# Optimization experiments

Measured on AMD Instinct MI355X. Metric: run time of the kernel, lower is better.

The kernel has to match this reference:

```python
import jax, jax.numpy as jnp
import numpy as np

N, E, B, H, F = 20000, 400000, 200, 10, 78
HID = H * F  # 780
SEQ, VOC, EMB, NF, KS = 1000, 26, 128, 32, 8
CONV_OUT = SEQ - KS + 1  # 993


def setup_inputs() -> dict:
    key = jax.random.key(0)
    ks = jax.random.split(key, 40)
    g = lambda i, shape, s=0.05: jax.random.normal(ks[i], shape, jnp.float32) * s
    inp = {
        "x": jax.random.normal(ks[0], (N, F), jnp.float32),
        "edge_index": jax.random.randint(ks[1], (2, E), 0, N),
        "batch": jnp.sort(jax.random.randint(ks[2], (N,), 0, B)),
        "target": jax.random.randint(ks[3], (B, SEQ), 0, VOC),
        # GATConv(78 -> 78, heads=10)
        "gat_W": g(4, (F, HID)),
        "gat_a_src": g(5, (H, F)),
        "gat_a_dst": g(6, (H, F)),
        "gat_b": g(7, (HID,)),
        # GCNConv(780 -> 780)
        "gcn_W": g(8, (HID, HID)),
        "gcn_b": g(9, (HID,)),
        # graph MLP head
        "fcg1_W": g(10, (HID, 1500)), "fcg1_b": g(11, (1500,)),
        "fcg2_W": g(12, (1500, 128)), "fcg2_b": g(13, (128,)),
        # protein branch
        "emb": g(14, (VOC, EMB)),
        "cW": g(15, (NF, EMB, KS)), "cb": g(16, (NF,)),
        "fxt_W": g(17, (NF * CONV_OUT, 128)), "fxt_b": g(18, (128,)),
        # fusion MLP
        "f1_W": g(19, (256, 1024)), "f1_b": g(20, (1024,)),
        "f2_W": g(21, (1024, 512)), "f2_b": g(22, (512,)),
        "f3_W": g(23, (512, 256)), "f3_b": g(24, (256,)),
        "f4_W": g(25, (256, 128)), "f4_b": g(26, (128,)),
        "o_W": g(27, (128, 1)), "o_b": g(28, (1,)),
    }
    return inp


def _graph_branch(x, edge_index, batch, gat_W, gat_a_src, gat_a_dst, gat_b,
                  gcn_W, gcn_b, fcg1_W, fcg1_b, fcg2_W, fcg2_b):
    n = x.shape[0]
    loops = jnp.arange(n)
    src = jnp.concatenate([edge_index[0], loops])  # add self loops (PyG default)
    dst = jnp.concatenate([edge_index[1], loops])
    # --- GATConv ---
    h = (x @ gat_W).reshape(n, H, F)  # [N,H,F]
    a_s = jnp.einsum("nhf,hf->nh", h, gat_a_src)
    a_d = jnp.einsum("nhf,hf->nh", h, gat_a_dst)
    e = jax.nn.leaky_relu(a_s[src] + a_d[dst], 0.2)  # [Etot,H]
    m = jax.ops.segment_max(e, dst, num_segments=n)
    ex = jnp.exp(e - m[dst])
    den = jax.ops.segment_sum(ex, dst, num_segments=n)
    alpha = ex / den[dst]
    agg = jax.ops.segment_sum(h[src] * alpha[:, :, None], dst, num_segments=n)
    x1 = jax.nn.relu(agg.reshape(n, HID) + gat_b)
    # --- GCNConv (sym norm with self loops) ---
    deg = jax.ops.segment_sum(jnp.ones_like(dst, jnp.float32), dst, num_segments=n)
    dinv = jax.lax.rsqrt(jnp.maximum(deg, 1.0))
    norm = dinv[src] * dinv[dst]
    h2 = x1 @ gcn_W
    x2 = jax.ops.segment_sum(h2[src] * norm[:, None], dst, num_segments=n) + gcn_b
    x2 = jax.nn.relu(x2)
    # --- global add pool + MLP ---
    xg = jax.ops.segment_sum(x2, batch, num_segments=B)
    xg = jax.nn.relu(xg @ fcg1_W + fcg1_b)  # dropout = identity (eval)
    return xg @ fcg2_W + fcg2_b


def _protein_branch(target, emb, cW, cb, fxt_W, fxt_b):
    et = emb[target]  # [B,SEQ,EMB]
    c = jax.lax.conv_general_dilated(
        et.transpose(0, 2, 1), cW, (1,), "VALID",
        dimension_numbers=("NCH", "OIH", "NCH"))  # [B,NF,993]
    c = c + cb[None, :, None]
    return c.reshape(c.shape[0], NF * CONV_OUT) @ fxt_W + fxt_b


def reference(x, edge_index, batch, target, gat_W, gat_a_src, gat_a_dst, gat_b,
              gcn_W, gcn_b, fcg1_W, fcg1_b, fcg2_W, fcg2_b, emb, cW, cb,
              fxt_W, fxt_b, f1_W, f1_b, f2_W, f2_b, f3_W, f3_b, f4_W, f4_b,
              o_W, o_b):
    xg = _graph_branch(x, edge_index, batch, gat_W, gat_a_src, gat_a_dst, gat_b,
                       gcn_W, gcn_b, fcg1_W, fcg1_b, fcg2_W, fcg2_b)
    xt = _protein_branch(target, emb, cW, cb, fxt_W, fxt_b)
    xc = jnp.concatenate([xg, xt], axis=1)  # [B,256]
    xc = jax.nn.relu(xc @ f1_W + f1_b)
    xc = jax.nn.relu(xc @ f2_W + f2_b)
    xc = jax.nn.relu(xc @ f3_W + f3_b)
    xc = jax.nn.relu(xc @ f4_W + f4_b)
    return xc @ o_W + o_b  # [B,1]
```

## Files before the change

kernel.cpp:

```cpp
#include <hip/hip_runtime.h>
#include <hip/hip_bf16.h>
#include <math.h>

typedef __hip_bfloat16 bf16;
typedef __attribute__((ext_vector_type(8))) short short8v;
typedef __attribute__((ext_vector_type(4))) float float4v;

#define NODES 20000
#define EDG   400000
#define ETOT  (EDG + NODES)
#define GB    200
#define HEADS 10
#define FD    78
#define HIDD  780
#define SEQL  1000
#define VOCS  26
#define EMBD  128
#define NFC   32
#define KSZ   8
#define COUT  993
#define KFXT  (NFC * COUT)

#define MPAD  20096
#define NPADB 896
#define KP1   96
#define KP2   800
#define HP    800
#define PNL   2
#define PF    400
#define MB2   208
#define FXT_KS 128


__device__ __forceinline__ float us2f(unsigned short u) {
  unsigned int i = ((unsigned int)u) << 16; float f; __builtin_memcpy(&f, &i, 4); return f;
}
__device__ __forceinline__ float b2f(bf16 v) { return __bfloat162float(v); }
__device__ __forceinline__ float ldany(const void* p, size_t i, int m) {
  if (m) return ((const float*)p)[i];
  return b2f(((const bf16*)p)[i]);
}
__device__ __forceinline__ bool nanf_(float v) { return v != v; }
__device__ __forceinline__ unsigned short f2us(float v) {
  bf16 b = __float2bfloat16(v); unsigned short u; __builtin_memcpy(&u, &b, 2); return u;
}

__global__ void k_detect(const void* x, int* diag) {
  int t = threadIdx.x;
  const unsigned short* u = (const unsigned short*)x;
  int hit = 0;
  for (int i = t; i < 4096; i += 256) {
    float v = us2f(u[i]);
    if (nanf_(v) || fabsf(v) > 1e6f) hit = 1;
  }
  if (hit) diag[1] = 1;
}

__global__ void k_pad_x(const void* x, bf16* xpad, const int* diag) {
  int idx = blockIdx.x * 256 + threadIdx.x;
  if (idx >= MPAD * KP1) return;
  int mode = diag[1];
  int m = idx / KP1, k = idx % KP1;
  float v = (m < NODES && k < FD) ? ldany(x, (size_t)m * FD + k, mode) : 0.f;
  xpad[idx] = __float2bfloat16(v);
}

__global__ void k_tr_gatw(const void* gw, bf16* Wt, const int* diag) {
  int idx = blockIdx.x * 256 + threadIdx.x;
  if (idx >= NPADB * KP1) return;
  int mode = diag[1];
  int n = idx / KP1, k = idx % KP1;
  float v = (n < HIDD && k < FD) ? ldany(gw, (size_t)k * HIDD + n, mode) : 0.f;
  Wt[idx] = __float2bfloat16(v);
}

__global__ void k_tr_gcnw(const void* gw, bf16* Wt, const int* diag) {
  int idx = blockIdx.x * 256 + threadIdx.x;
  if (idx >= NPADB * KP2) return;
  int mode = diag[1];
  int n = idx / KP2, k = idx % KP2;
  float v = (n < HIDD && k < HIDD) ? ldany(gw, (size_t)k * HIDD + n, mode) : 0.f;
  Wt[idx] = __float2bfloat16(v);
}

__global__ void k_zero_x1pad(bf16* x1p) {
  int i = blockIdx.x * 256 + threadIdx.x;
  if (i < (MPAD - NODES) * KP2)
    x1p[(size_t)NODES * KP2 + i] = __float2bfloat16(0.f);
}

#define MT 128
#define NT 128
#define BK 32
#define LP 40
__global__ __launch_bounds__(256) void k_gemm_mfma(const bf16* A, int lda,
                                                   const bf16* Bt, int ldb,
                                                   bf16* C, int ldc, int Ncap,
                                                   int M, int Kp) {
  __shared__ __align__(16) bf16 As[MT * LP];
  __shared__ __align__(16) bf16 Bs[NT * LP];
  int t = threadIdx.x;
  int lane = t & 63, w = t >> 6;
  int wr = (w >> 1) * 64, wc = (w & 1) * 64;
  int quad = lane >> 4, mr = lane & 15;
  int m0 = blockIdx.y * MT, n0 = blockIdx.x * NT;
  float4v acc[4][4];
#pragma unroll
  for (int i = 0; i < 4; ++i)
#pragma unroll
    for (int j = 0; j < 4; ++j) acc[i][j] = (float4v){0.f, 0.f, 0.f, 0.f};

  for (int kc = 0; kc < Kp; kc += BK) {
#pragma unroll
    for (int i = 0; i < 4; ++i) {
      int c = t + i * 256;
      int row = c >> 3, col = (c & 7) * 4;
      *(uint2*)&As[row * LP + col] =
          *(const uint2*)&A[(size_t)(m0 + row) * lda + kc + col];
      *(uint2*)&Bs[row * LP + col] =
          *(const uint2*)&Bt[(size_t)(n0 + row) * ldb + kc + col];
    }
    __syncthreads();
    short8v af[4], bfr[4];
#pragma unroll
    for (int i = 0; i < 4; ++i)
      af[i] = *(const short8v*)&As[(wr + i * 16 + mr) * LP + quad * 8];
#pragma unroll
    for (int j = 0; j < 4; ++j)
      bfr[j] = *(const short8v*)&Bs[(wc + j * 16 + mr) * LP + quad * 8];
#pragma unroll
    for (int i = 0; i < 4; ++i)
#pragma unroll
      for (int j = 0; j < 4; ++j)
        acc[i][j] = __builtin_amdgcn_mfma_f32_16x16x32_bf16(af[i], bfr[j], acc[i][j], 0, 0, 0);
    __syncthreads();
  }
#pragma unroll
  for (int i = 0; i < 4; ++i) {
    int gm0 = m0 + wr + i * 16 + quad * 4;
#pragma unroll
    for (int j = 0; j < 4; ++j) {
      int gn = n0 + wc + j * 16 + mr;
      if (gn >= Ncap) continue;
#pragma unroll
      for (int r = 0; r < 4; ++r) {
        int gm = gm0 + r;
        if (gm < M) C[(size_t)gm * ldc + gn] = __float2bfloat16(acc[i][j][r]);
      }
    }
  }
}

#define MLP_NT 64
#define MLP_BK 32
#define MLP_MT 208
#define MLP_LP 40
__global__ __launch_bounds__(256) void k_mlp_mfma(const void* A, int lda, const void* Bw,
                                                  const void* bias, float* out, int ostride,
                                                  int ooff, int M, int Nn, int K,
                                                  int ksplit, int aRelu, int aBf16,
                                                  const int* diag) {
  __shared__ __align__(16) bf16 As[MLP_MT * MLP_LP];
  __shared__ __align__(16) bf16 Bs[MLP_NT * MLP_LP];
  int mode = diag[1];
  int t = threadIdx.x;
  int lane = t & 63, w = t >> 6;
  int quad = lane >> 4, mr = lane & 15;
  int n0 = blockIdx.x * MLP_NT;
  int kz = blockIdx.y;
  int nchunks = (K + MLP_BK - 1) / MLP_BK;
  int cpk = (nchunks + ksplit - 1) / ksplit;
  int c0 = kz * cpk, c1 = c0 + cpk;
  if (c1 > nchunks) c1 = nchunks;
  float4v acc[13];
#pragma unroll
  for (int i = 0; i < 13; ++i) acc[i] = (float4v){0.f, 0.f, 0.f, 0.f};

  for (int c = c0; c < c1; ++c) {
    int k0 = c * MLP_BK;
    if (aBf16) {
      const bf16* Ab = (const bf16*)A;
      for (int e = t; e < MLP_MT * 4; e += 256) {
        int row = e >> 2, c8 = (e & 3) * 8;
        int gk = k0 + c8;
        if (row < M && gk + 7 < K) {
          *(uint4*)&As[row * MLP_LP + c8] = *(const uint4*)&Ab[(size_t)row * lda + gk];
        } else {
#pragma unroll
          for (int kk = 0; kk < 8; ++kk) {
            float v = (row < M && gk + kk < K) ? b2f(Ab[(size_t)row * lda + gk + kk]) : 0.f;
            As[row * MLP_LP + c8 + kk] = __float2bfloat16(v);
          }
        }
      }
    } else {
      const float* Af = (const float*)A;
      for (int e = t; e < MLP_MT * 8; e += 256) {
        int row = e >> 3, c4 = (e & 7) * 4;
        int gk = k0 + c4;
        float4 v4 = {0.f, 0.f, 0.f, 0.f};
        if (row < M) {
          if (gk + 3 < K) {
            v4 = *(const float4*)&Af[(size_t)row * lda + gk];
          } else {
            v4.x = (gk + 0 < K) ? Af[(size_t)row * lda + gk + 0] : 0.f;
            v4.y = (gk + 1 < K) ? Af[(size_t)row * lda + gk + 1] : 0.f;
            v4.z = (gk + 2 < K) ? Af[(size_t)row * lda + gk + 2] : 0.f;
            v4.w = (gk + 3 < K) ? Af[(size_t)row * lda + gk + 3] : 0.f;
          }
        }
        if (aRelu) {
          v4.x = fmaxf(v4.x, 0.f); v4.y = fmaxf(v4.y, 0.f);
          v4.z = fmaxf(v4.z, 0.f); v4.w = fmaxf(v4.w, 0.f);
        }
        bf16* dst = &As[row * MLP_LP + c4];
        dst[0] = __float2bfloat16(v4.x); dst[1] = __float2bfloat16(v4.y);
        dst[2] = __float2bfloat16(v4.z); dst[3] = __float2bfloat16(v4.w);
      }
    }
    for (int e = t; e < MLP_NT * MLP_BK; e += 256) {
      int k = e >> 6, col = e & 63;
      int gk = k0 + k, gn = n0 + col;
      float v = (gn < Nn && gk < K) ? ldany(Bw, (size_t)gk * Nn + gn, mode) : 0.f;
      Bs[col * MLP_LP + k] = __float2bfloat16(v);
    }
    __syncthreads();
    short8v bf = *(const short8v*)&Bs[(w * 16 + mr) * MLP_LP + quad * 8];
#pragma unroll
    for (int i = 0; i < 13; ++i) {
      short8v af = *(const short8v*)&As[(i * 16 + mr) * MLP_LP + quad * 8];
      acc[i] = __builtin_amdgcn_mfma_f32_16x16x32_bf16(af, bf, acc[i], 0, 0, 0);
    }
    __syncthreads();
  }
  int gn = n0 + w * 16 + mr;
  if (gn >= Nn) return;
  float bs = (kz == 0) ? ldany(bias, gn, mode) : 0.f;
#pragma unroll
  for (int i = 0; i < 13; ++i) {
    int gm0 = i * 16 + quad * 4;
#pragma unroll
    for (int r = 0; r < 4; ++r) {
      int gm = gm0 + r;
      if (gm >= M) break;
      float v = acc[i][r] + bs;
      float* op = &out[(size_t)gm * ostride + ooff + gn];
      if (ksplit == 1) *op = v;
      else atomicAdd(op, v);
    }
  }
}

__global__ __launch_bounds__(256) void k_fxt(const bf16* cT, const void* Bw,
                                             float* part, const int* diag) {
  __shared__ __align__(16) bf16 As[MLP_MT * MLP_LP];
  __shared__ __align__(16) bf16 Bs[MLP_NT * MLP_LP];
  int mode = diag[1];
  int t = threadIdx.x;
  int lane = t & 63, w = t >> 6;
  int quad = lane >> 4, mr = lane & 15;
  int n0 = blockIdx.x * MLP_NT;
  int kz = blockIdx.y;
  int nchunks = KFXT / MLP_BK;
  int cpk = (nchunks + FXT_KS - 1) / FXT_KS;
  int c0 = kz * cpk, c1 = c0 + cpk;
  if (c1 > nchunks) c1 = nchunks;
  float4v acc[13];
#pragma unroll
  for (int i = 0; i < 13; ++i) acc[i] = (float4v){0.f, 0.f, 0.f, 0.f};

  for (int c = c0; c < c1; ++c) {
    int k0 = c * MLP_BK;
    for (int e = t; e < 32 * 52; e += 256) {
      int kk = e / 52, bq = e % 52;
      uint2 u = *(const uint2*)&cT[(size_t)(k0 + kk) * MB2 + bq * 4];
      unsigned short* ap = (unsigned short*)As;
      int mb = bq * 4;
      ap[(mb + 0) * MLP_LP + kk] = (unsigned short)(u.x & 0xffffu);
      ap[(mb + 1) * MLP_LP + kk] = (unsigned short)(u.x >> 16);
      ap[(mb + 2) * MLP_LP + kk] = (unsigned short)(u.y & 0xffffu);
      ap[(mb + 3) * MLP_LP + kk] = (unsigned short)(u.y >> 16);
    }
    for (int e = t; e < MLP_NT * MLP_BK; e += 256) {
      int k = e >> 6, col = e & 63;
      float v = ldany(Bw, (size_t)(k0 + k) * 128 + (n0 + col), mode);
      Bs[col * MLP_LP + k] = __float2bfloat16(v);
    }
    __syncthreads();
    short8v bf = *(const short8v*)&Bs[(w * 16 + mr) * MLP_LP + quad * 8];
#pragma unroll
    for (int i = 0; i < 13; ++i) {
      short8v af = *(const short8v*)&As[(i * 16 + mr) * MLP_LP + quad * 8];
      acc[i] = __builtin_amdgcn_mfma_f32_16x16x32_bf16(af, bf, acc[i], 0, 0, 0);
    }
    __syncthreads();
  }
  int gnl = n0 + w * 16 + mr;
#pragma unroll
  for (int i = 0; i < 13; ++i) {
#pragma unroll
    for (int r = 0; r < 4; ++r) {
      int gm = i * 16 + quad * 4 + r;
      part[((size_t)kz * MB2 + gm) * 128 + gnl] = acc[i][r];
    }
  }
}

__global__ __launch_bounds__(128) void k_fxt_red(const float* part, const void* bias,
                                                 float* xc, const int* diag) {
  int gm = blockIdx.x, n = threadIdx.x;
  int mode = diag[1];
  float s = 0.f;
  for (int kz = 0; kz < FXT_KS; ++kz)
    s += part[((size_t)kz * MB2 + gm) * 128 + n];
  xc[(size_t)gm * 256 + 128 + n] = s + ldany(bias, n, mode);
}

__global__ void k_prep_ws(const void* gat_W, const void* a_src, const void* a_dst,
                          float* Ws, float* Wd, const int* diag) {
  int idx = blockIdx.x * 256 + threadIdx.x;
  if (idx >= FD * HEADS) return;
  int mode = diag[1];
  int k = idx / HEADS, hd = idx % HEADS;
  float s = 0.f, d = 0.f;
  for (int f = 0; f < FD; ++f) {
    float w = ldany(gat_W, (size_t)k * HIDD + hd * FD + f, mode);
    s += w * ldany(a_src, (size_t)hd * FD + f, mode);
    d += w * ldany(a_dst, (size_t)hd * FD + f, mode);
  }
  Ws[k * HEADS + hd] = s;
  Wd[k * HEADS + hd] = d;
}

__global__ void k_prep_mtab(const void* emb, const void* cW, float* Mtab, const int* diag) {
  int idx = blockIdx.x * 256 + threadIdx.x;
  if (idx >= NFC * KSZ * VOCS) return;
  int mode = diag[1];
  int o = idx / (KSZ * VOCS);
  int r = idx % (KSZ * VOCS);
  int k = r / VOCS, v = r % VOCS;
  float acc = 0.f;
  for (int i = 0; i < EMBD; ++i)
    acc += ldany(emb, (size_t)v * EMBD + i, mode) * ldany(cW, ((size_t)o * EMBD + i) * KSZ + k, mode);
  Mtab[idx] = acc;
}

__global__ __launch_bounds__(256) void k_asd(const void* x, const float* Ws, const float* Wd,
                                             float* a_s, float* a_d, const int* diag) {
  __shared__ unsigned short xs[256 * FD];
  __shared__ float ws_sh[FD * HEADS], wd_sh[FD * HEADS];
  int mode = diag[1];
  int nb = blockIdx.x * 256, t = threadIdx.x;
  for (int e = t; e < FD * HEADS; e += 256) { ws_sh[e] = Ws[e]; wd_sh[e] = Wd[e]; }
  for (int e = t; e < 256 * FD; e += 256) {
    int r = e / FD, c = e % FD;
    int gn = nb + r;
    float xv = (gn < NODES) ? ldany(x, (size_t)gn * FD + c, mode) : 0.f;
    xs[e] = f2us(xv);
  }
  __syncthreads();
  int n = nb + t;
  if (n >= NODES) return;
  float as[HEADS], ad[HEADS];
#pragma unroll
  for (int hd = 0; hd < HEADS; ++hd) { as[hd] = 0.f; ad[hd] = 0.f; }
  for (int f = 0; f < FD; ++f) {
    float xv = us2f(xs[t * FD + f]);
#pragma unroll
    for (int hd = 0; hd < HEADS; ++hd) {
      as[hd] += xv * ws_sh[f * HEADS + hd];
      ad[hd] += xv * wd_sh[f * HEADS + hd];
    }
  }
#pragma unroll
  for (int hd = 0; hd < HEADS; ++hd) {
    a_s[n * HEADS + hd] = as[hd];
    a_d[n * HEADS + hd] = ad[hd];
  }
}

__global__ void k_count(const int* ei, int* cnt, int* diag) {
  int e = blockIdx.x * 256 + threadIdx.x;
  if (e >= ETOT) return;
  int d = (e < EDG) ? ei[EDG + e] : (e - EDG);
  if ((unsigned)d >= NODES) { atomicOr(diag, 8192); d = 0; }
  atomicAdd(&cnt[d], 1);
}

__global__ __launch_bounds__(1024) void k_scan(const int* cnt, int* rowstart) {
  __shared__ int wsum[16];
  __shared__ int carry;
  int t = threadIdx.x;
  int lane = t & 63, wid = t >> 6;
  if (t == 0) carry = 0;
  __syncthreads();
  for (int c = 0; c < (NODES + 1023) / 1024; ++c) {
    int i = c * 1024 + t;
    int orig = (i < NODES) ? cnt[i] : 0;
    int v = orig;
#pragma unroll
    for (int off = 1; off < 64; off <<= 1) {
      int u = __shfl_up(v, off, 64);
      if (lane >= off) v += u;
    }
    if (lane == 63) wsum[wid] = v;
    __syncthreads();
    if (t == 0) {
      int s = carry;
      for (int j = 0; j < 16; ++j) { int tmp = wsum[j]; wsum[j] = s; s += tmp; }
      carry = s;
    }
    __syncthreads();
    if (i < NODES) rowstart[i] = v - orig + wsum[wid];
    __syncthreads();
  }
  if (t == 0) rowstart[NODES] = carry;
}

__global__ void k_dinv(const int* cnt, float* dinv) {
  int n = blockIdx.x * 256 + threadIdx.x;
  if (n >= NODES) return;
  int d = cnt[n];
  dinv[n] = rsqrtf((float)(d > 0 ? d : 1));
}

__global__ void k_scatter(const int* ei, const int* rowstart, int* cur, int* es_src,
                          int* diag) {
  int e = blockIdx.x * 256 + threadIdx.x;
  if (e >= ETOT) return;
  int s, d;
  if (e < EDG) { s = ei[e]; d = ei[EDG + e]; } else { s = e - EDG; d = s; }
  if ((unsigned)d >= NODES) { atomicOr(diag, 8192); d = 0; }
  if ((unsigned)s >= NODES) { atomicOr(diag, 8192); s = 0; }
  int pos = rowstart[d] + atomicAdd(&cur[d], 1);
  if ((unsigned)pos < (unsigned)ETOT) es_src[pos] = s;
  else atomicOr(diag, 1);
}

__global__ void k_csrchk(const int* cnt, const int* cur, const int* rowst, int* diag) {
  int n = blockIdx.x * 256 + threadIdx.x;
  if (n < NODES && cur[n] != cnt[n]) atomicOr(diag, 1);
  if (n == 0 && rowst[NODES] != ETOT) atomicOr(diag, 1);
}

__global__ void k_bseg(const int* batch, int* bstart, int* diag) {
  int i = blockIdx.x * 256 + threadIdx.x;
  if (i >= NODES) return;
  int bi = batch[i];
  if ((unsigned)bi >= GB) { atomicOr(diag, 8192); bi = GB - 1; }
  int bp;
  if (i == 0) bp = -1;
  else {
    bp = batch[i - 1];
    if ((unsigned)bp >= GB) bp = GB - 1;
  }
  for (int b = bp + 1; b <= bi; ++b) bstart[b] = i;
  if (i == NODES - 1)
    for (int b = bi + 1; b <= GB; ++b) bstart[b] = NODES;
}

__global__ __launch_bounds__(64) void k_alpha(const int* es_src, const int* rowst,
                                              const float* a_s, const float* a_d,
                                              float* alpha, int* diag) {
  int d = blockIdx.x, lane = threadIdx.x;
  int start = rowst[d], end = rowst[d + 1];
  float ad[HEADS];
#pragma unroll
  for (int j = 0; j < HEADS; ++j) ad[j] = a_d[d * HEADS + j];
  float mx[HEADS];
#pragma unroll
  for (int j = 0; j < HEADS; ++j) mx[j] = -INFINITY;
  for (int base = start; base < end; base += 64) {
    int ce = base + lane;
    if (ce < end) {
      int s = es_src[ce];
      if ((unsigned)s >= NODES) { atomicOr(diag, 1); s = 0; }
#pragma unroll
      for (int j = 0; j < HEADS; ++j) {
        float v = a_s[s * HEADS + j] + ad[j];
        v = v > 0.f ? v : 0.2f * v;
        mx[j] = fmaxf(mx[j], v);
      }
    }
  }
#pragma unroll
  for (int j = 0; j < HEADS; ++j)
    for (int off = 1; off < 64; off <<= 1) mx[j] = fmaxf(mx[j], __shfl_xor(mx[j], off, 64));
  float den[HEADS];
#pragma unroll
  for (int j = 0; j < HEADS; ++j) den[j] = 0.f;
  for (int base = start; base < end; base += 64) {
    int ce = base + lane;
    if (ce < end) {
      int s = es_src[ce];
      if ((unsigned)s >= NODES) s = 0;
#pragma unroll
      for (int j = 0; j < HEADS; ++j) {
        float v = a_s[s * HEADS + j] + ad[j];
        v = v > 0.f ? v : 0.2f * v;
        den[j] += expf(v - mx[j]);
      }
    }
  }
#pragma unroll
  for (int j = 0; j < HEADS; ++j)
    for (int off = 1; off < 64; off <<= 1) den[j] += __shfl_xor(den[j], off, 64);
  if (lane == 0 && (nanf_(den[0]) || nanf_(den[HEADS - 1]))) atomicOr(diag, 2);
  for (int base = start; base < end; base += 64) {
    int ce = base + lane;
    if (ce < end) {
      int s = es_src[ce];
      if ((unsigned)s >= NODES) s = 0;
#pragma unroll
      for (int j = 0; j < HEADS; ++j) {
        float v = a_s[s * HEADS + j] + ad[j];
        v = v > 0.f ? v : 0.2f * v;
        alpha[(size_t)ce * HEADS + j] = expf(v - mx[j]) / den[j];
      }
    }
  }
}

__global__ __launch_bounds__(64) void k_gatg(const int* es_src, const int* rowst,
                                             const float* alpha, const bf16* h,
                                             const void* gat_b, bf16* x1, int* diag) {
  __shared__ int ssc[64];
  __shared__ float alw[64 * HEADS];
  int bid = blockIdx.x;
  int p = bid & (PNL - 1), d = bid >> 1;
  int lane = threadIdx.x;
  int mode = diag[1];
  int start = rowst[d], end = rowst[d + 1];
  int fb = p * PF + lane * 8;
  int hr = fb / FD;
  int hA = hr > HEADS - 1 ? HEADS - 1 : hr;
  int hB = hr + 1 > HEADS - 1 ? HEADS - 1 : hr + 1;
  int bnd = (hr + 1) * FD - fb;
  float acc[8];
#pragma unroll
  for (int k = 0; k < 8; ++k) acc[k] = 0.f;
  for (int base = start; base < end; base += 64) {
    int ce = base + lane;
    if (ce < end) {
      int s = es_src[ce];
      if ((unsigned)s >= NODES) { atomicOr(diag, 1); s = 0; }
      ssc[lane] = s;
#pragma unroll
      for (int j = 0; j < HEADS; ++j) alw[lane * HEADS + j] = alpha[(size_t)ce * HEADS + j];
    }
    __syncthreads();
    int cnt2 = end - base; if (cnt2 > 64) cnt2 = 64;
    if (lane < 50) {
      for (int e = 0; e < cnt2; ++e) {
        int ss = ssc[e];
        float aA = alw[e * HEADS + hA];
        float aB = alw[e * HEADS + hB];
        uint4 u = *(const uint4*)(h + (size_t)ss * HP + fb);
        unsigned int uw[4] = {u.x, u.y, u.z, u.w};
#pragma unroll
        for (int k = 0; k < 4; ++k) {
          float wl = (2 * k < bnd) ? aA : aB;
          float wh = (2 * k + 1 < bnd) ? aA : aB;
          acc[2 * k]     += wl * us2f((unsigned short)(uw[k] & 0xffffu));
          acc[2 * k + 1] += wh * us2f((unsigned short)(uw[k] >> 16));
        }
      }
    }
    __syncthreads();
  }
  if (lane < 50) {
    if (nanf_(acc[0]) || nanf_(acc[7])) atomicOr(diag, 8);
    unsigned short o[8];
#pragma unroll
    for (int k = 0; k < 8; ++k) {
      int f = fb + k;
      float v = 0.f;
      if (f < HIDD) v = fmaxf(acc[k] + ldany(gat_b, f, mode), 0.f);
      o[k] = f2us(v);
    }
    uint4 pack;
    __builtin_memcpy(&pack, o, 16);
    *(uint4*)(x1 + (size_t)d * KP2 + fb) = pack;
  }
}

__global__ __launch_bounds__(64) void k_gcng(const int* es_src, const int* rowst,
                                             const float* dinv, const bf16* h2,
                                             const void* gcn_b, bf16* x2b, int* diag) {
  __shared__ int ssc[64];
  __shared__ float nw[64];
  int bid = blockIdx.x;
  int p = bid & (PNL - 1), d = bid >> 1;
  int lane = threadIdx.x;
  int mode = diag[1];
  int start = rowst[d], end = rowst[d + 1];
  float dd = dinv[d];
  int fb = p * PF + lane * 8;
  float acc[8];
#pragma unroll
  for (int k = 0; k < 8; ++k) acc[k] = 0.f;
  for (int base = start; base < end; base += 64) {
    int ce = base + lane;
    if (ce < end) {
      int s = es_src[ce];
      if ((unsigned)s >= NODES) { atomicOr(diag, 1); s = 0; }
      ssc[lane] = s;
      nw[lane] = dinv[s] * dd;
    }
    __syncthreads();
    int cnt2 = end - base; if (cnt2 > 64) cnt2 = 64;
    if (lane < 50) {
      for (int e = 0; e < cnt2; ++e) {
        int ss = ssc[e];
        float nv = nw[e];
        uint4 u = *(const uint4*)(h2 + (size_t)ss * HP + fb);
        unsigned int uw[4] = {u.x, u.y, u.z, u.w};
#pragma unroll
        for (int k = 0; k < 4; ++k) {
          acc[2 * k]     += nv * us2f((unsigned short)(uw[k] & 0xffffu));
          acc[2 * k + 1] += nv * us2f((unsigned short)(uw[k] >> 16));
        }
      }
    }
    __syncthreads();
  }
  if (lane < 50) {
    if (nanf_(acc[0]) || nanf_(acc[7])) atomicOr(diag, 16);
    unsigned short o[8];
#pragma unroll
    for (int k = 0; k < 8; ++k) {
      int f = fb + k;
      float v = 0.f;
      if (f < HIDD) v = fmaxf(acc[k] + ldany(gcn_b, f, mode), 0.f);
      o[k] = f2us(v);
    }
    uint4 pack;
    __builtin_memcpy(&pack, o, 16);
    *(uint4*)(x2b + (size_t)d * HP + fb) = pack;
  }
}

__global__ __launch_bounds__(256) void k_pool(const bf16* x2b, const int* bstart,
                                              float* xg_pool) {
  int b = blockIdx.x, t = threadIdx.x;
  if (t >= 195) return;
  int r0 = bstart[b], r1 = bstart[b + 1];
  int fb = t * 4;
  float4 acc = {0.f, 0.f, 0.f, 0.f};
  for (int r = r0; r < r1; ++r) {
    uint2 u = *(const uint2*)(x2b + (size_t)r * HP + fb);
    acc.x += us2f((unsigned short)(u.x & 0xffffu));
    acc.y += us2f((unsigned short)(u.x >> 16));
    acc.z += us2f((unsigned short)(u.y & 0xffffu));
    acc.w += us2f((unsigned short)(u.y >> 16));
  }
  *(float4*)&xg_pool[(size_t)b * HIDD + fb] = acc;
}

__global__ __launch_bounds__(256) void k_convT(const int* target, const float* Mtab,
                                               const void* cb, bf16* cT, int* diag) {
  __shared__ int tg[GB * 40];
  __shared__ float Mt[KSZ * VOCS];
  int tt0 = blockIdx.x * 32, o = blockIdx.y, t = threadIdx.x;
  int mode = diag[1];
  for (int e = t; e < KSZ * VOCS; e += 256)
    Mt[e] = Mtab[(o * KSZ + e / VOCS) * VOCS + (e % VOCS)];
  for (int e = t; e < GB * 40; e += 256) {
    int b = e / 40, q = e % 40;
    int pos = tt0 + q;
    int tv = (pos < SEQL) ? target[b * SEQL + pos] : 0;
    if ((unsigned)tv >= VOCS) { atomicOr(diag, 8192); tv = 0; }
    tg[e] = tv;
  }
  __syncthreads();
  float cbv = ldany(cb, o, mode);
  for (int e = t; e < 32 * MB2; e += 256) {
    int tt = e / MB2, b = e % MB2;
    int gtt = tt0 + tt;
    if (gtt >= COUT) continue;
    float acc = 0.f;
    if (b < GB) {
#pragma unroll
      for (int k = 0; k < KSZ; ++k)
        acc += Mt[k * VOCS + tg[b * 40 + tt + k]];
      acc += cbv;
      if (nanf_(acc)) atomicOr(diag, 4096);
    }
    cT[((size_t)o * COUT + gtt) * MB2 + b] = __float2bfloat16(b < GB ? acc : 0.f);
  }
}

__global__ __launch_bounds__(64) void k_out(const float* xf4, const void* o_W,
                                            const void* o_b, void* outp, const int* diag) {
  int b = blockIdx.x, lane = threadIdx.x;
  int mode = diag[1];
  float a0 = fmaxf(xf4[b * 128 + lane], 0.f);
  float a1 = fmaxf(xf4[b * 128 + 64 + lane], 0.f);
  float v = a0 * ldany(o_W, lane, mode) + a1 * ldany(o_W, 64 + lane, mode);
  for (int off = 32; off; off >>= 1) v += __shfl_down(v, off, 64);
  if (lane == 0) {
    float r = v + ldany(o_b, 0, mode);
    int dg = diag[0];
    if (dg) r = 256.f * (1 + mode) + 8.f * (float)(__ffs(dg) - 1);
    else if (nanf_(r)) r = 200.f + 100.f * mode;
    if (mode) ((float*)outp)[b] = r;
    else ((bf16*)outp)[b] = __float2bfloat16(r);
  }
}

extern "C" void kernel_launch(void* const* d_in, const int* in_sizes, int n_in,
                              void* d_out, int out_size, void* d_ws, size_t ws_size,
                              hipStream_t stream) {
  const void* x       = d_in[0];
  const int*  ei      = (const int*)d_in[1];
  const int*  batch   = (const int*)d_in[2];
  const int*  target  = (const int*)d_in[3];
  const void* gat_W   = d_in[4];
  const void* a_src   = d_in[5];
  const void* a_dst   = d_in[6];
  const void* gat_b   = d_in[7];
  const void* gcn_W   = d_in[8];
  const void* gcn_b   = d_in[9];
  const void* fcg1_W  = d_in[10];
  const void* fcg1_b  = d_in[11];
  const void* fcg2_W  = d_in[12];
  const void* fcg2_b  = d_in[13];
  const void* emb     = d_in[14];
  const void* cW      = d_in[15];
  const void* cb      = d_in[16];
  const void* fxt_W   = d_in[17];
  const void* fxt_b   = d_in[18];
  const void* f1_W    = d_in[19];
  const void* f1_b    = d_in[20];
  const void* f2_W    = d_in[21];
  const void* f2_b    = d_in[22];
  const void* f3_W    = d_in[23];
  const void* f3_b    = d_in[24];
  const void* f4_W    = d_in[25];
  const void* f4_b    = d_in[26];
  const void* o_W     = d_in[27];
  const void* o_b     = d_in[28];

  char* w = (char*)d_ws;
  size_t off = 0;
  auto alloc = [&](size_t bytes) -> void* {
    void* p = w + off;
    off = (off + bytes + 255) & ~(size_t)255;
    return p;
  };
  bf16*  h_buf   = (bf16*)alloc((size_t)NODES * HP * 2);
  bf16*  x1p     = (bf16*)alloc((size_t)MPAD * KP2 * 2);
  bf16*  xpad    = (bf16*)alloc((size_t)MPAD * KP1 * 2);
  bf16*  gatWt   = (bf16*)alloc((size_t)NPADB * KP1 * 2);
  bf16*  gcnWt   = (bf16*)alloc((size_t)NPADB * KP2 * 2);
  float* a_s     = (float*)alloc((size_t)NODES * HEADS * 4);
  float* a_d     = (float*)alloc((size_t)NODES * HEADS * 4);
  float* alpha   = (float*)alloc((size_t)ETOT * HEADS * 4);
  float* Ws      = (float*)alloc(FD * HEADS * 4);
  float* Wd      = (float*)alloc(FD * HEADS * 4);
  float* Mtab    = (float*)alloc(NFC * KSZ * VOCS * 4);
  int*   rowst   = (int*)alloc((NODES + 1) * 4);
  float* dinv    = (float*)alloc(NODES * 4);
  int*   bstart  = (int*)alloc((GB + 1) * 4);
  bf16*  cT      = (bf16*)alloc((size_t)KFXT * MB2 * 2);
  float* part    = (float*)alloc((size_t)FXT_KS * MB2 * 128 * 4);
  size_t zoff = off;
  int*   cnt     = (int*)alloc(NODES * 4);
  int*   cur     = (int*)alloc(NODES * 4);
  int*   es_src  = (int*)alloc((size_t)ETOT * 4);
  float* xg_pool = (float*)alloc((size_t)GB * HIDD * 4);
  float* xg1     = (float*)alloc((size_t)GB * 1500 * 4);
  float* xc      = (float*)alloc((size_t)GB * 256 * 4);
  float* xf1     = (float*)alloc((size_t)GB * 1024 * 4);
  float* xf2     = (float*)alloc((size_t)GB * 512 * 4);
  float* xf3     = (float*)alloc((size_t)GB * 256 * 4);
  float* xf4     = (float*)alloc((size_t)GB * 128 * 4);
  int*   diag    = (int*)alloc(2 * 4);
  size_t zlen = off - zoff;

  bf16* x2b = x1p;

  hipMemsetAsync(w + zoff, 0, zlen, stream);

  k_detect<<<1, 256, 0, stream>>>(x, diag);

  k_pad_x<<<(MPAD * KP1 + 255) / 256, 256, 0, stream>>>(x, xpad, diag);
  k_tr_gatw<<<(NPADB * KP1 + 255) / 256, 256, 0, stream>>>(gat_W, gatWt, diag);
  k_tr_gcnw<<<(NPADB * KP2 + 255) / 256, 256, 0, stream>>>(gcn_W, gcnWt, diag);
  k_zero_x1pad<<<((MPAD - NODES) * KP2 + 255) / 256, 256, 0, stream>>>(x1p);

  k_prep_ws<<<(FD * HEADS + 255) / 256, 256, 0, stream>>>(gat_W, a_src, a_dst, Ws, Wd, diag);
  k_prep_mtab<<<(NFC * KSZ * VOCS + 255) / 256, 256, 0, stream>>>(emb, cW, Mtab, diag);

  k_gemm_mfma<<<dim3(NPADB / NT, MPAD / MT), 256, 0, stream>>>(
      xpad, KP1, gatWt, KP1, h_buf, HP, HP, NODES, KP1);
  k_asd<<<(NODES + 255) / 256, 256, 0, stream>>>(x, Ws, Wd, a_s, a_d, diag);

  k_count<<<(ETOT + 255) / 256, 256, 0, stream>>>(ei, cnt, diag);
  k_scan<<<1, 1024, 0, stream>>>(cnt, rowst);
  k_dinv<<<(NODES + 255) / 256, 256, 0, stream>>>(cnt, dinv);
  k_scatter<<<(ETOT + 255) / 256, 256, 0, stream>>>(ei, rowst, cur, es_src, diag);
  k_csrchk<<<(NODES + 255) / 256, 256, 0, stream>>>(cnt, cur, rowst, diag);
  k_bseg<<<(NODES + 255) / 256, 256, 0, stream>>>(batch, bstart, diag);

  k_alpha<<<NODES, 64, 0, stream>>>(es_src, rowst, a_s, a_d, alpha, diag);
  k_gatg<<<NODES * PNL, 64, 0, stream>>>(es_src, rowst, alpha, h_buf, gat_b, x1p, diag);

  k_gemm_mfma<<<dim3(NPADB / NT, MPAD / MT), 256, 0, stream>>>(
      x1p, KP2, gcnWt, KP2, h_buf, HP, HP, NODES, KP2);

  k_gcng<<<NODES * PNL, 64, 0, stream>>>(es_src, rowst, dinv, h_buf, gcn_b, x2b, diag);
  k_pool<<<GB, 256, 0, stream>>>(x2b, bstart, xg_pool);

  k_convT<<<dim3((COUT + 31) / 32, NFC), 256, 0, stream>>>(target, Mtab, cb, cT, diag);
  k_fxt<<<dim3(2, FXT_KS), 256, 0, stream>>>(cT, fxt_W, part, diag);
  k_fxt_red<<<GB, 128, 0, stream>>>(part, fxt_b, xc, diag);

  k_mlp_mfma<<<dim3(24, 4), 256, 0, stream>>>(xg_pool, HIDD, fcg1_W, fcg1_b,
                                              xg1, 1500, 0, GB, 1500, HIDD, 4, 0, 0, diag);
  k_mlp_mfma<<<dim3(2, 16), 256, 0, stream>>>(xg1, 1500, fcg2_W, fcg2_b,
                                              xc, 256, 0, GB, 128, 1500, 16, 1, 0, diag);
  k_mlp_mfma<<<dim3(16, 4), 256, 0, stream>>>(xc, 256, f1_W, f1_b,
                                              xf1, 1024, 0, GB, 1024, 256, 4, 0, 0, diag);
  k_mlp_mfma<<<dim3(8, 8), 256, 0, stream>>>(xf1, 1024, f2_W, f2_b,
                                             xf2, 512, 0, GB, 512, 1024, 8, 1, 0, diag);
  k_mlp_mfma<<<dim3(4, 8), 256, 0, stream>>>(xf2, 512, f3_W, f3_b,
                                             xf3, 256, 0, GB, 256, 512, 8, 1, 0, diag);
  k_mlp_mfma<<<dim3(2, 8), 256, 0, stream>>>(xf3, 256, f4_W, f4_b,
                                             xf4, 128, 0, GB, 128, 256, 8, 1, 0, diag);
  k_out<<<GB, 64, 0, stream>>>(xf4, o_W, o_b, d_out, diag);
}
```

Before: 909.3 us.

## Aggregate raw features per head before GAT projection, then apply per-head GEMM

Reorders the GAT computation: instead of projecting x to 780-dim h and gathering h rows per edge, it aggregates the 78-dim input features weighted by the per-head alpha into a [N,10,96] buffer, then runs a per-head MFMA GEMM with a fused bias and ReLU. This cuts per-edge gather traffic from 780 bf16 values to 78 input values, at the cost of a 10-head accumulator per lane and a larger intermediate buffer. The cT/part buffers are aliased onto the new aggx buffer to reuse memory, and the x1 pad columns are now zeroed explicitly.

```diff
diff --git a/kernel.cpp b/kernel.cpp
--- a/kernel.cpp
+++ b/kernel.cpp
@@ -23,13 +23,14 @@
 
 #define MPAD  20096
 #define NPADB 896
-#define KP1   96
 #define KP2   800
 #define HP    800
 #define PNL   2
 #define PF    400
 #define MB2   208
 #define FXT_KS 128
+#define HK    96
+#define AGS   960
 
 
 __device__ __forceinline__ float us2f(unsigned short u) {
@@ -56,24 +57,6 @@
   if (hit) diag[1] = 1;
 }
 
-__global__ void k_pad_x(const void* x, bf16* xpad, const int* diag) {
-  int idx = blockIdx.x * 256 + threadIdx.x;
-  if (idx >= MPAD * KP1) return;
-  int mode = diag[1];
-  int m = idx / KP1, k = idx % KP1;
-  float v = (m < NODES && k < FD) ? ldany(x, (size_t)m * FD + k, mode) : 0.f;
-  xpad[idx] = __float2bfloat16(v);
-}
-
-__global__ void k_tr_gatw(const void* gw, bf16* Wt, const int* diag) {
-  int idx = blockIdx.x * 256 + threadIdx.x;
-  if (idx >= NPADB * KP1) return;
-  int mode = diag[1];
-  int n = idx / KP1, k = idx % KP1;
-  float v = (n < HIDD && k < FD) ? ldany(gw, (size_t)k * HIDD + n, mode) : 0.f;
-  Wt[idx] = __float2bfloat16(v);
-}
-
 __global__ void k_tr_gcnw(const void* gw, bf16* Wt, const int* diag) {
   int idx = blockIdx.x * 256 + threadIdx.x;
   if (idx >= NPADB * KP2) return;
@@ -83,10 +66,29 @@
   Wt[idx] = __float2bfloat16(v);
 }
 
+__global__ void k_prep_wt2(const void* gw, bf16* Wt2, const int* diag) {
+  int idx = blockIdx.x * 256 + threadIdx.x;
+  if (idx >= HEADS * 128 * HK) return;
+  int mode = diag[1];
+  int h = idx / (128 * HK);
+  int r = idx % (128 * HK);
+  int n = r / HK, k = r % HK;
+  float v = (n < FD && k < FD) ? ldany(gw, (size_t)k * HIDD + h * FD + n, mode) : 0.f;
+  Wt2[idx] = __float2bfloat16(v);
+}
+
 __global__ void k_zero_x1pad(bf16* x1p) {
   int i = blockIdx.x * 256 + threadIdx.x;
-  if (i < (MPAD - NODES) * KP2)
+  int nr = (MPAD - NODES) * KP2;
+  if (i < nr) {
     x1p[(size_t)NODES * KP2 + i] = __float2bfloat16(0.f);
+  } else {
+    int j = i - nr;
+    if (j < NODES * 20) {
+      int d = j / 20, c = HIDD + (j % 20);
+      x1p[(size_t)d * KP2 + c] = __float2bfloat16(0.f);
+    }
+  }
 }
 
 #define MT 128
@@ -146,6 +148,69 @@
       for (int r = 0; r < 4; ++r) {
         int gm = gm0 + r;
         if (gm < M) C[(size_t)gm * ldc + gn] = __float2bfloat16(acc[i][j][r]);
+      }
+    }
+  }
+}
+
+__global__ __launch_bounds__(256) void k_hgemm(const bf16* aggx, const bf16* Wt2,
+                                               const void* gat_b, bf16* x1,
+                                               const int* diag) {
+  __shared__ __align__(16) bf16 As[MT * LP];
+  __shared__ __align__(16) bf16 Bs[NT * LP];
+  int t = threadIdx.x;
+  int lane = t & 63, w = t >> 6;
+  int wr = (w >> 1) * 64, wc = (w & 1) * 64;
+  int quad = lane >> 4, mr = lane & 15;
+  int m0 = blockIdx.x * MT, h = blockIdx.y;
+  int mode = diag[1];
+  const bf16* A = aggx + (size_t)h * HK;
+  const bf16* Bt = Wt2 + (size_t)h * 128 * HK;
+  float4v acc[4][4];
+#pragma unroll
+  for (int i = 0; i < 4; ++i)
+#pragma unroll
+    for (int j = 0; j < 4; ++j) acc[i][j] = (float4v){0.f, 0.f, 0.f, 0.f};
+
+  for (int kc = 0; kc < HK; kc += BK) {
+#pragma unroll
+    for (int i = 0; i < 4; ++i) {
+      int c = t + i * 256;
+      int row = c >> 3, col = (c & 7) * 4;
+      *(uint2*)&As[row * LP + col] =
+          *(const uint2*)&A[(size_t)(m0 + row) * AGS + kc + col];
+      *(uint2*)&Bs[row * LP + col] =
+          *(const uint2*)&Bt[(size_t)row * HK + kc + col];
+    }
+    __syncthreads();
+    short8v af[4], bfr[4];
+#pragma unroll
+    for (int i = 0; i < 4; ++i)
+      af[i] = *(const short8v*)&As[(wr + i * 16 + mr) * LP + quad * 8];
+#pragma unroll
+    for (int j = 0; j < 4; ++j)
+      bfr[j] = *(const short8v*)&Bs[(wc + j * 16 + mr) * LP + quad * 8];
+#pragma unroll
+    for (int i = 0; i < 4; ++i)
+#pragma unroll
+      for (int j = 0; j < 4; ++j)
+        acc[i][j] = __builtin_amdgcn_mfma_f32_16x16x32_bf16(af[i], bfr[j], acc[i][j], 0, 0, 0);
+    __syncthreads();
+  }
+#pragma unroll
+  for (int i = 0; i < 4; ++i) {
+    int gm0 = m0 + wr + i * 16 + quad * 4;
+#pragma unroll
+    for (int j = 0; j < 4; ++j) {
+      int gn = wc + j * 16 + mr;
+      if (gn >= FD) continue;
+      float bs = ldany(gat_b, h * FD + gn, mode);
+#pragma unroll
+      for (int r = 0; r < 4; ++r) {
+        int gm = gm0 + r;
+        if (gm < NODES)
+          x1[(size_t)gm * KP2 + h * FD + gn] =
+              __float2bfloat16(fmaxf(acc[i][j][r] + bs, 0.f));
       }
     }
   }
@@ -521,24 +586,18 @@
   }
 }
 
-__global__ __launch_bounds__(64) void k_gatg(const int* es_src, const int* rowst,
-                                             const float* alpha, const bf16* h,
-                                             const void* gat_b, bf16* x1, int* diag) {
+__global__ __launch_bounds__(64) void k_gatx(const int* es_src, const int* rowst,
+                                             const float* alpha, const void* x,
+                                             bf16* aggx, int* diag) {
   __shared__ int ssc[64];
   __shared__ float alw[64 * HEADS];
-  int bid = blockIdx.x;
-  int p = bid & (PNL - 1), d = bid >> 1;
-  int lane = threadIdx.x;
+  int d = blockIdx.x, lane = threadIdx.x;
   int mode = diag[1];
   int start = rowst[d], end = rowst[d + 1];
-  int fb = p * PF + lane * 8;
-  int hr = fb / FD;
-  int hA = hr > HEADS - 1 ? HEADS - 1 : hr;
-  int hB = hr + 1 > HEADS - 1 ? HEADS - 1 : hr + 1;
-  int bnd = (hr + 1) * FD - fb;
-  float acc[8];
-#pragma unroll
-  for (int k = 0; k < 8; ++k) acc[k] = 0.f;
+  int f0 = 2 * lane;
+  float acc[HEADS][2];
+#pragma unroll
+  for (int j = 0; j < HEADS; ++j) { acc[j][0] = 0.f; acc[j][1] = 0.f; }
   for (int base = start; base < end; base += 64) {
     int ce = base + lane;
     if (ce < end) {
@@ -550,37 +609,40 @@
     }
     __syncthreads();
     int cnt2 = end - base; if (cnt2 > 64) cnt2 = 64;
-    if (lane < 50) {
+    if (lane < 39) {
       for (int e = 0; e < cnt2; ++e) {
         int ss = ssc[e];
-        float aA = alw[e * HEADS + hA];
-        float aB = alw[e * HEADS + hB];
-        uint4 u = *(const uint4*)(h + (size_t)ss * HP + fb);
-        unsigned int uw[4] = {u.x, u.y, u.z, u.w};
-#pragma unroll
-        for (int k = 0; k < 4; ++k) {
-          float wl = (2 * k < bnd) ? aA : aB;
-          float wh = (2 * k + 1 < bnd) ? aA : aB;
-          acc[2 * k]     += wl * us2f((unsigned short)(uw[k] & 0xffffu));
-          acc[2 * k + 1] += wh * us2f((unsigned short)(uw[k] >> 16));
+        float xv0, xv1;
+        if (mode) {
+          const float* xf = (const float*)x;
+          xv0 = xf[(size_t)ss * FD + f0];
+          xv1 = xf[(size_t)ss * FD + f0 + 1];
+        } else {
+          unsigned int u = *(const unsigned int*)((const unsigned short*)x +
+                                                  (size_t)ss * FD + f0);
+          xv0 = us2f((unsigned short)(u & 0xffffu));
+          xv1 = us2f((unsigned short)(u >> 16));
+        }
+        const float* al = &alw[e * HEADS];
+#pragma unroll
+        for (int j = 0; j < HEADS; ++j) {
+          acc[j][0] += al[j] * xv0;
+          acc[j][1] += al[j] * xv1;
         }
       }
     }
     __syncthreads();
   }
-  if (lane < 50) {
-    if (nanf_(acc[0]) || nanf_(acc[7])) atomicOr(diag, 8);
-    unsigned short o[8];
-#pragma unroll
-    for (int k = 0; k < 8; ++k) {
-      int f = fb + k;
-      float v = 0.f;
-      if (f < HIDD) v = fmaxf(acc[k] + ldany(gat_b, f, mode), 0.f);
-      o[k] = f2us(v);
-    }
-    uint4 pack;
-    __builtin_memcpy(&pack, o, 16);
-    *(uint4*)(x1 + (size_t)d * KP2 + fb) = pack;
+  if (lane < 48) {
+    if (lane < 39 && (nanf_(acc[0][0]) || nanf_(acc[HEADS - 1][1]))) atomicOr(diag, 8);
+    size_t rb = (size_t)d * AGS;
+#pragma unroll
+    for (int h = 0; h < HEADS; ++h) {
+      unsigned short o0 = (f0 < FD) ? f2us(acc[h][0]) : (unsigned short)0;
+      unsigned short o1 = (f0 + 1 < FD) ? f2us(acc[h][1]) : (unsigned short)0;
+      unsigned int pack = (unsigned int)o0 | ((unsigned int)o1 << 16);
+      *(unsigned int*)(aggx + rb + h * HK + f0) = pack;
+    }
   }
 }
 
@@ -750,8 +812,8 @@
   };
   bf16*  h_buf   = (bf16*)alloc((size_t)NODES * HP * 2);
   bf16*  x1p     = (bf16*)alloc((size_t)MPAD * KP2 * 2);
-  bf16*  xpad    = (bf16*)alloc((size_t)MPAD * KP1 * 2);
-  bf16*  gatWt   = (bf16*)alloc((size_t)NPADB * KP1 * 2);
+  bf16*  aggx    = (bf16*)alloc((size_t)MPAD * AGS * 2);
+  bf16*  gatWt2  = (bf16*)alloc((size_t)HEADS * 128 * HK * 2);
   bf16*  gcnWt   = (bf16*)alloc((size_t)NPADB * KP2 * 2);
   float* a_s     = (float*)alloc((size_t)NODES * HEADS * 4);
   float* a_d     = (float*)alloc((size_t)NODES * HEADS * 4);
@@ -762,8 +824,6 @@
   int*   rowst   = (int*)alloc((NODES + 1) * 4);
   float* dinv    = (float*)alloc(NODES * 4);
   int*   bstart  = (int*)alloc((GB + 1) * 4);
-  bf16*  cT      = (bf16*)alloc((size_t)KFXT * MB2 * 2);
-  float* part    = (float*)alloc((size_t)FXT_KS * MB2 * 128 * 4);
   size_t zoff = off;
   int*   cnt     = (int*)alloc(NODES * 4);
   int*   cur     = (int*)alloc(NODES * 4);
@@ -779,21 +839,21 @@
   size_t zlen = off - zoff;
 
   bf16* x2b = x1p;
+  bf16*  cT   = (bf16*)aggx;
+  size_t cTb  = ((size_t)KFXT * MB2 * 2 + 255) & ~(size_t)255;
+  float* part = (float*)((char*)aggx + cTb);
 
   hipMemsetAsync(w + zoff, 0, zlen, stream);
 
   k_detect<<<1, 256, 0, stream>>>(x, diag);
 
-  k_pad_x<<<(MPAD * KP1 + 255) / 256, 256, 0, stream>>>(x, xpad, diag);
-  k_tr_gatw<<<(NPADB * KP1 + 255) / 256, 256, 0, stream>>>(gat_W, gatWt, diag);
   k_tr_gcnw<<<(NPADB * KP2 + 255) / 256, 256, 0, stream>>>(gcn_W, gcnWt, diag);
-  k_zero_x1pad<<<((MPAD - NODES) * KP2 + 255) / 256, 256, 0, stream>>>(x1p);
+  k_prep_wt2<<<(HEADS * 128 * HK + 255) / 256, 256, 0, stream>>>(gat_W, gatWt2, diag);
+  k_zero_x1pad<<<((MPAD - NODES) * KP2 + NODES * 20 + 255) / 256, 256, 0, stream>>>(x1p);
 
   k_prep_ws<<<(FD * HEADS + 255) / 256, 256, 0, stream>>>(gat_W, a_src, a_dst, Ws, Wd, diag);
   k_prep_mtab<<<(NFC * KSZ * VOCS + 255) / 256, 256, 0, stream>>>(emb, cW, Mtab, diag);
 
-  k_gemm_mfma<<<dim3(NPADB / NT, MPAD / MT), 256, 0, stream>>>(
-      xpad, KP1, gatWt, KP1, h_buf, HP, HP, NODES, KP1);
   k_asd<<<(NODES + 255) / 256, 256, 0, stream>>>(x, Ws, Wd, a_s, a_d, diag);
 
   k_count<<<(ETOT + 255) / 256, 256, 0, stream>>>(ei, cnt, diag);
@@ -804,7 +864,8 @@
   k_bseg<<<(NODES + 255) / 256, 256, 0, stream>>>(batch, bstart, diag);
 
   k_alpha<<<NODES, 64, 0, stream>>>(es_src, rowst, a_s, a_d, alpha, diag);
-  k_gatg<<<NODES * PNL, 64, 0, stream>>>(es_src, rowst, alpha, h_buf, gat_b, x1p, diag);
+  k_gatx<<<NODES, 64, 0, stream>>>(es_src, rowst, alpha, x, aggx, diag);
+  k_hgemm<<<dim3(MPAD / MT, HEADS), 256, 0, stream>>>(aggx, gatWt2, gat_b, x1p, diag);
 
   k_gemm_mfma<<<dim3(NPADB / NT, MPAD / MT), 256, 0, stream>>>(
       x1p, KP2, gcnWt, KP2, h_buf, HP, HP, NODES, KP2);
```

Result: faster. 879.3 us (-3.3%).
